# Kernel optimization log

Measured on AMD Instinct MI355X. Metric: run time of the kernel, lower is better.

The kernel has to match this reference:

```python
import jax, jax.numpy as jnp
import numpy as np

NEG_SLOPE = 0.01  # torch F.leaky_relu default
N_USER = 100000
N_ITEM = 100000
N_EDGE = 640000
D = 128
N_LAYERS = 3  # 1 input + num_hidden_layers(1) + 1 output layer


def setup_inputs() -> dict:
    key = jax.random.key(0)
    ks = jax.random.split(key, 10)
    scale = 1.0 / np.sqrt(D)
    return {
        "h_user": jax.random.normal(ks[0], (N_USER, D), dtype=jnp.float32),
        "h_item": jax.random.normal(ks[1], (N_ITEM, D), dtype=jnp.float32),
        # W[layer, etype] : etype 0 = user-follows->user, 1 = user-clicks->item, 2 = item-clicked_by->user
        "W": jax.random.normal(ks[2], (N_LAYERS, 3, D, D), dtype=jnp.float32) * scale,
        "b": jnp.zeros((N_LAYERS, 3, D), dtype=jnp.float32),
        "follows_src": jax.random.randint(ks[3], (N_EDGE,), 0, N_USER, dtype=jnp.int32),
        "follows_dst": jax.random.randint(ks[4], (N_EDGE,), 0, N_USER, dtype=jnp.int32),
        "clicks_src": jax.random.randint(ks[5], (N_EDGE,), 0, N_USER, dtype=jnp.int32),
        "clicks_dst": jax.random.randint(ks[6], (N_EDGE,), 0, N_ITEM, dtype=jnp.int32),
        "cb_src": jax.random.randint(ks[7], (N_EDGE,), 0, N_ITEM, dtype=jnp.int32),
        "cb_dst": jax.random.randint(ks[8], (N_EDGE,), 0, N_USER, dtype=jnp.int32),
    }


def _etype_conv(h_src, W, b, src, dst, n_dst):
    """Per-etype Linear on src nodes, copy_u gather, mean-aggregate at dst."""
    Wh = h_src @ W + b                     # [N_src, D] dense transform (once per node)
    msg = Wh[src]                          # [E, D] gather
    s = jax.ops.segment_sum(msg, dst, num_segments=n_dst)
    cnt = jax.ops.segment_sum(jnp.ones((src.shape[0],), dtype=Wh.dtype), dst, num_segments=n_dst)
    return s / jnp.maximum(cnt, 1.0)[:, None]  # mean; isolated nodes -> 0


def _rgcn_forward(h_user, h_item, W, b, follows_src, follows_dst,
                  clicks_src, clicks_dst, cb_src, cb_dst):
    hu, hi = h_user, h_item
    for l in range(N_LAYERS):
        # per-etype mean aggregation, then cross-etype 'sum' (DGL multi_update_all)
        agg_u = (_etype_conv(hu, W[l, 0], b[l, 0], follows_src, follows_dst, N_USER)
                 + _etype_conv(hi, W[l, 2], b[l, 2], cb_src, cb_dst, N_USER))
        agg_i = _etype_conv(hu, W[l, 1], b[l, 1], clicks_src, clicks_dst, N_ITEM)
        hu = jax.nn.leaky_relu(agg_u, NEG_SLOPE)
        hi = jax.nn.leaky_relu(agg_i, NEG_SLOPE)
    return jnp.stack([hu, hi])  # [2, 100000, 128]


def reference(h_user, h_item, W, b, follows_src, follows_dst,
              clicks_src, clicks_dst, cb_src, cb_dst):
    return _rgcn_forward(h_user, h_item, W, b, follows_src, follows_dst,
                         clicks_src, clicks_dst, cb_src, cb_dst)
```

## Files before the change

kernel.cpp:

```cpp
#include <hip/hip_runtime.h>

typedef unsigned short u16;
typedef _Float16 f16;
typedef __attribute__((ext_vector_type(8))) _Float16 f16x8;
typedef __attribute__((ext_vector_type(4))) float f32x4;

#define D 128

__global__ __launch_bounds__(256) void k_convert(const float* __restrict__ in,
                                                 u16* __restrict__ out, int n8) {
  int i = blockIdx.x * 256 + threadIdx.x;
  if (i >= n8) return;
  const float4* ip = (const float4*)in;
  float4 a = ip[i * 2], b = ip[i * 2 + 1];
  f16x8 v = {(f16)a.x, (f16)a.y, (f16)a.z, (f16)a.w,
             (f16)b.x, (f16)b.y, (f16)b.z, (f16)b.w};
  *(f16x8*)(out + (size_t)i * 8) = v;
}

__global__ __launch_bounds__(256) void k_convW(const float* __restrict__ W,
                                               u16* __restrict__ Wt, int total) {
  int idx = blockIdx.x * 256 + threadIdx.x;
  if (idx >= total) return;
  int mat = idx >> 14;
  int k = (idx >> 7) & 127;
  int n = idx & 127;
  f16 v = (f16)W[idx];
  ((f16*)Wt)[(size_t)mat * 16384 + n * 128 + k] = v;
}

__global__ __launch_bounds__(256) void k_countpos(
    const int* __restrict__ fd, const int* __restrict__ cd,
    const int* __restrict__ cbd, int* __restrict__ cnt, u16* __restrict__ pos,
    int NU, int NI, int nf, int nc, int ncb, int S) {
  int e = blockIdx.x * 256 + threadIdx.x;
  int d;
  if (e < nf)
    d = fd[e];
  else if (e < nf + nc)
    d = NU + cd[e - nf];
  else if (e < nf + nc + ncb)
    d = NU + NI + cbd[e - nf - nc];
  else
    return;
  int p = atomicAdd(&cnt[d * S], 1);
  pos[e] = (u16)p;
}

__global__ __launch_bounds__(256) void k_scanA(const int* __restrict__ cnt,
                                               int* __restrict__ part, int n, int S) {
  int t = threadIdx.x;
  int idx = blockIdx.x * 1024 + t * 4;
  int s = 0;
#pragma unroll
  for (int j = 0; j < 4; ++j)
    if (idx + j < n) s += cnt[(idx + j) * S];
  for (int off = 1; off < 64; off <<= 1) s += __shfl_down(s, off, 64);
  __shared__ int ws[4];
  if ((t & 63) == 0) ws[t >> 6] = s;
  __syncthreads();
  if (t == 0) part[blockIdx.x] = ws[0] + ws[1] + ws[2] + ws[3];
}

__global__ __launch_bounds__(1024) void k_scanB(int* __restrict__ part, int n_part) {
  __shared__ int sh[1024];
  int t = threadIdx.x;
  int v = (t < n_part) ? part[t] : 0;
  sh[t] = v;
  __syncthreads();
  for (int off = 1; off < 1024; off <<= 1) {
    int u = (t >= off) ? sh[t - off] : 0;
    __syncthreads();
    sh[t] += u;
    __syncthreads();
  }
  if (t < n_part) part[t] = sh[t] - v;
}

__global__ __launch_bounds__(256) void k_scanC(const int* __restrict__ cnt,
                                               const int* __restrict__ part,
                                               int* __restrict__ rs,
                                               int n, int total, int S) {
  int t = threadIdx.x;
  int idx = blockIdx.x * 1024 + t * 4;
  int v0 = 0, v1 = 0, v2 = 0, v3 = 0;
  if (idx < n) v0 = cnt[idx * S];
  if (idx + 1 < n) v1 = cnt[(idx + 1) * S];
  if (idx + 2 < n) v2 = cnt[(idx + 2) * S];
  if (idx + 3 < n) v3 = cnt[(idx + 3) * S];
  int s = v0 + v1 + v2 + v3;
  int inc = s;
  int lane = t & 63, w = t >> 6;
  for (int off = 1; off < 64; off <<= 1) {
    int u = __shfl_up(inc, off, 64);
    if (lane >= off) inc += u;
  }
  __shared__ int ws[4];
  if (lane == 63) ws[w] = inc;
  __syncthreads();
  int woff = 0;
  for (int i = 0; i < w; ++i) woff += ws[i];
  int ex = part[blockIdx.x] + woff + inc - s;
  int4 r;
  r.x = ex;
  r.y = ex + v0;
  r.z = r.y + v1;
  r.w = r.z + v2;
  if (idx + 3 < n)
    *(int4*)(rs + idx) = r;
  else {
    if (idx < n) rs[idx] = r.x;
    if (idx + 1 < n) rs[idx + 1] = r.y;
    if (idx + 2 < n) rs[idx + 2] = r.z;
    if (idx + 3 < n) rs[idx + 3] = r.w;
  }
  if (blockIdx.x == 0 && t == 0) rs[n] = total;
}

__global__ __launch_bounds__(256) void k_fillpos(
    const int* __restrict__ fs, const int* __restrict__ fd,
    const int* __restrict__ cs, const int* __restrict__ cd,
    const int* __restrict__ cbs, const int* __restrict__ cbd,
    const int* __restrict__ rs, const u16* __restrict__ pos,
    int* __restrict__ csr, int NU, int NI, int nf, int nc, int ncb) {
  int e = blockIdx.x * 256 + threadIdx.x;
  int d, s;
  if (e < nf) {
    d = fd[e];
    s = fs[e];
  } else if (e < nf + nc) {
    d = NU + cd[e - nf];
    s = cs[e - nf];
  } else if (e < nf + nc + ncb) {
    d = NU + NI + cbd[e - nf - nc];
    s = cbs[e - nf - nc] + NU;
  } else
    return;
  csr[rs[d] + (int)pos[e]] = s;
}

__global__ __launch_bounds__(256) void k_agg3(
    const u16* __restrict__ h_all, const int* __restrict__ csr,
    const int* __restrict__ rs, u16* __restrict__ M_all, int N3) {
  int wave = (blockIdx.x * 256 + threadIdx.x) >> 6;
  int lane = threadIdx.x & 63;
  int l16 = lane & 15;
  int w = wave * 4 + (lane >> 4);
  bool valid = w < N3;
  int wc = valid ? w : 0;
  int e = rs[wc];
  int en = valid ? rs[wc + 1] : 0;
  int deg = en - e;
  f16x8 acc0 = {0, 0, 0, 0, 0, 0, 0, 0};
  f16x8 acc1 = {0, 0, 0, 0, 0, 0, 0, 0};
  const char* hb = (const char*)h_all;
  unsigned loff = (unsigned)l16 * 16u;

  while (__any(e < en)) {
    bool a0 = e < en, a1 = e + 1 < en, a2 = e + 2 < en, a3 = e + 3 < en;
    int s0 = a0 ? csr[e] : 0;
    int s1 = a1 ? csr[e + 1] : 0;
    int s2 = a2 ? csr[e + 2] : 0;
    int s3 = a3 ? csr[e + 3] : 0;
    f16x8 v0 = {0, 0, 0, 0, 0, 0, 0, 0}, v1 = {0, 0, 0, 0, 0, 0, 0, 0};
    f16x8 v2 = {0, 0, 0, 0, 0, 0, 0, 0}, v3 = {0, 0, 0, 0, 0, 0, 0, 0};
    if (a0) v0 = *(const f16x8*)(hb + ((unsigned)s0 * 256u + loff));
    if (a1) v1 = *(const f16x8*)(hb + ((unsigned)s1 * 256u + loff));
    if (a2) v2 = *(const f16x8*)(hb + ((unsigned)s2 * 256u + loff));
    if (a3) v3 = *(const f16x8*)(hb + ((unsigned)s3 * 256u + loff));
    acc0 += v0;
    acc1 += v1;
    acc0 += v2;
    acc1 += v3;
    e += 4;
  }

  if (valid) {
    float invf = deg > 0 ? 1.0f / (float)deg : 0.f;
    f16 hinv = (f16)invf;
    f16x8 t = acc0 + acc1;
    f16x8 r = t * hinv;
    *(f16x8*)((char*)M_all + ((unsigned)wc * 256u + loff)) = r;
  }
}

template <int NE, int OUTF32>
__device__ __forceinline__ void gemm_body(
    const u16* __restrict__ mA, const u16* __restrict__ mBp,
    const u16* __restrict__ wtA, const u16* __restrict__ wtB,
    const float* __restrict__ bA, const float* __restrict__ bB,
    const int* __restrict__ rsA, const int* __restrict__ rsB,
    u16* __restrict__ o16, float* __restrict__ o32, int M, int blk) {
  int tid = threadIdx.x, lane = tid & 63, w = tid >> 6;
  int lr = lane & 15;
  int lk = (lane >> 4) * 8;
  long row0 = (long)blk * 128 + w * 32;

  f32x4 acc[2][8];
#pragma unroll
  for (int rt = 0; rt < 2; rt++)
#pragma unroll
    for (int n = 0; n < 8; n++) acc[rt][n] = (f32x4){0.f, 0.f, 0.f, 0.f};

#pragma unroll
  for (int e = 0; e < NE; ++e) {
    const f16* mm = (const f16*)((e == 0) ? mA : mBp);
    const f16* Wg = (const f16*)((e == 0) ? wtA : wtB);
#pragma unroll
    for (int ks = 0; ks < 4; ++ks) {
      int k0 = ks * 32 + lk;
      f16x8 bf[8];
#pragma unroll
      for (int n = 0; n < 8; n++) bf[n] = *(const f16x8*)(Wg + (n * 16 + lr) * D + k0);
#pragma unroll
      for (int rt = 0; rt < 2; rt++) {
        long r = row0 + rt * 16 + lr;
        if (r >= M) r = M - 1;
        f16x8 af = *(const f16x8*)(mm + r * D + k0);
#pragma unroll
        for (int n = 0; n < 8; n++)
          acc[rt][n] = __builtin_amdgcn_mfma_f32_16x16x32_f16(af, bf[n], acc[rt][n], 0, 0, 0);
      }
    }
  }

  float bAr[8], bBr[8];
#pragma unroll
  for (int n = 0; n < 8; n++) {
    bAr[n] = bA[n * 16 + lr];
    bBr[n] = (NE == 2) ? bB[n * 16 + lr] : 0.f;
  }

#pragma unroll
  for (int rt = 0; rt < 2; rt++) {
    long rbase = row0 + rt * 16 + (lane >> 4) * 4;
#pragma unroll
    for (int i = 0; i < 4; i++) {
      long r = rbase + i;
      if (r < M) {
        bool mAok = rsA[r + 1] > rsA[r];
        bool mBok = (NE == 2) && (rsB[r + 1] > rsB[r]);
#pragma unroll
        for (int n = 0; n < 8; n++) {
          int col = n * 16 + lr;
          float v = acc[rt][n][i];
          if (mAok) v += bAr[n];
          if (mBok) v += bBr[n];
          v = v > 0.f ? v : 0.01f * v;
          if (OUTF32)
            o32[r * D + col] = v;
          else
            ((f16*)o16)[r * D + col] = (f16)v;
        }
      }
    }
  }
}

template <int OUTF32>
__global__ __launch_bounds__(256) void k_gemm2(
    const u16* __restrict__ M_all, const u16* __restrict__ Wl,
    const float* __restrict__ bl, const int* __restrict__ rs_all,
    u16* __restrict__ h_all, float* __restrict__ out,
    int NU, int NI, int nbI) {
  if ((int)blockIdx.x < nbI) {
    gemm_body<1, OUTF32>(M_all + (size_t)NU * D, nullptr,
                         Wl + 16384, nullptr,
                         bl + D, nullptr,
                         rs_all + NU, nullptr,
                         h_all + (size_t)NU * D, out + (size_t)NU * D, NI,
                         blockIdx.x);
  } else {
    gemm_body<2, OUTF32>(M_all, M_all + (size_t)(NU + NI) * D,
                         Wl, Wl + 2 * 16384,
                         bl, bl + 2 * D,
                         rs_all, rs_all + NU + NI,
                         h_all, out, NU, blockIdx.x - nbI);
  }
}

extern "C" void kernel_launch(void* const* d_in, const int* in_sizes, int n_in,
                              void* d_out, int out_size, void* d_ws, size_t ws_size,
                              hipStream_t stream) {
  const float* h_user = (const float*)d_in[0];
  const float* h_item = (const float*)d_in[1];
  const float* W = (const float*)d_in[2];
  const float* bb = (const float*)d_in[3];
  const int* f_src = (const int*)d_in[4];
  const int* f_dst = (const int*)d_in[5];
  const int* c_src = (const int*)d_in[6];
  const int* c_dst = (const int*)d_in[7];
  const int* cb_src = (const int*)d_in[8];
  const int* cb_dst = (const int*)d_in[9];

  const int NU = in_sizes[0] / D;
  const int NI = in_sizes[1] / D;
  const int nEf = in_sizes[4], nEc = in_sizes[6], nEcb = in_sizes[8];
  const int N3 = NU + NI + NU;
  const int nE = nEf + nEc + nEcb;

  size_t fixed = (size_t)(N3 + 1) * 4 + 1024 * 4 + (size_t)9 * 16384 * 2 +
                 (size_t)nE * 4 + (size_t)nE * 2 +
                 (size_t)(NU + NI) * D * 2 + (size_t)N3 * D * 2 + 4096;
  int S = (fixed + (size_t)N3 * 64 <= ws_size) ? 16 : 1;

  char* p = (char*)d_ws;
  auto alloc = [&](size_t bytes) {
    char* r = p;
    p += (bytes + 255) & ~(size_t)255;
    return r;
  };
  int* cnt_pad = (int*)alloc((size_t)N3 * 4 * S);
  int* rs_all = (int*)alloc((size_t)(N3 + 1) * 4);
  int* part = (int*)alloc(1024 * 4);
  u16* Wtg = (u16*)alloc((size_t)9 * 16384 * 2);
  int* csr_all = (int*)alloc((size_t)nE * 4);
  u16* pos = (u16*)alloc((size_t)nE * 2);
  u16* h_all = (u16*)alloc((size_t)(NU + NI) * D * 2);
  u16* M_all = (u16*)alloc((size_t)N3 * D * 2);

  hipMemsetAsync(cnt_pad, 0, (size_t)N3 * 4 * S, stream);

  k_convert<<<(NU * D / 8 + 255) / 256, 256, 0, stream>>>(h_user, h_all, NU * D / 8);
  k_convert<<<(NI * D / 8 + 255) / 256, 256, 0, stream>>>(h_item, h_all + (size_t)NU * D,
                                                          NI * D / 8);
  k_convW<<<(9 * 16384 + 255) / 256, 256, 0, stream>>>(W, Wtg, 9 * 16384);

  k_countpos<<<(nE + 255) / 256, 256, 0, stream>>>(f_dst, c_dst, cb_dst, cnt_pad, pos,
                                                   NU, NI, nEf, nEc, nEcb, S);

  int n_part = (N3 + 1023) / 1024;
  k_scanA<<<n_part, 256, 0, stream>>>(cnt_pad, part, N3, S);
  k_scanB<<<1, 1024, 0, stream>>>(part, n_part);
  k_scanC<<<n_part, 256, 0, stream>>>(cnt_pad, part, rs_all, N3, nE, S);

  k_fillpos<<<(nE + 255) / 256, 256, 0, stream>>>(f_src, f_dst, c_src, c_dst,
                                                  cb_src, cb_dst, rs_all, pos,
                                                  csr_all, NU, NI, nEf, nEc, nEcb);

  int nbI = (NI + 127) / 128;
  int nbU = (NU + 127) / 128;
  int agg_blocks = ((N3 + 3) / 4 + 3) / 4;

  for (int l = 0; l < 3; ++l) {
    const u16* Wl = Wtg + (size_t)l * 3 * 16384;
    const float* bl = bb + (size_t)l * 3 * D;

    k_agg3<<<agg_blocks, 256, 0, stream>>>(h_all, csr_all, rs_all, M_all, N3);

    if (l < 2)
      k_gemm2<0><<<nbI + nbU, 256, 0, stream>>>(M_all, Wl, bl, rs_all, h_all,
                                                (float*)d_out, NU, NI, nbI);
    else
      k_gemm2<1><<<nbI + nbU, 256, 0, stream>>>(M_all, Wl, bl, rs_all, h_all,
                                                (float*)d_out, NU, NI, nbI);
  }
}
```

Baseline: 577.7 us.

## Fuse preprocessing kernels, unroll gather by eight, vectorize GEMM epilogue stores

Merges the fp32-to-fp16 conversion, weight transpose and degree-count kernels into one launch with block-range dispatch, which removes launch gaps. The aggregation loop now issues eight neighbor-row loads per iteration instead of four, so more memory requests are in flight. The MFMA operands are swapped so each lane holds four consecutive columns of one row, which lets the epilogue read bias as float4 and write vectorized float4/f16x4 stores instead of scattered scalar stores. Costs are more registers in the gather loop and a few extra predicated loads for low-degree nodes.

```diff
diff --git a/kernel.cpp b/kernel.cpp
--- a/kernel.cpp
+++ b/kernel.cpp
@@ -2,49 +2,54 @@
 
 typedef unsigned short u16;
 typedef _Float16 f16;
+typedef __attribute__((ext_vector_type(4))) _Float16 f16x4;
 typedef __attribute__((ext_vector_type(8))) _Float16 f16x8;
 typedef __attribute__((ext_vector_type(4))) float f32x4;
 
 #define D 128
 
-__global__ __launch_bounds__(256) void k_convert(const float* __restrict__ in,
-                                                 u16* __restrict__ out, int n8) {
-  int i = blockIdx.x * 256 + threadIdx.x;
-  if (i >= n8) return;
-  const float4* ip = (const float4*)in;
-  float4 a = ip[i * 2], b = ip[i * 2 + 1];
-  f16x8 v = {(f16)a.x, (f16)a.y, (f16)a.z, (f16)a.w,
-             (f16)b.x, (f16)b.y, (f16)b.z, (f16)b.w};
-  *(f16x8*)(out + (size_t)i * 8) = v;
-}
-
-__global__ __launch_bounds__(256) void k_convW(const float* __restrict__ W,
-                                               u16* __restrict__ Wt, int total) {
-  int idx = blockIdx.x * 256 + threadIdx.x;
-  if (idx >= total) return;
-  int mat = idx >> 14;
-  int k = (idx >> 7) & 127;
-  int n = idx & 127;
-  f16 v = (f16)W[idx];
-  ((f16*)Wt)[(size_t)mat * 16384 + n * 128 + k] = v;
-}
-
-__global__ __launch_bounds__(256) void k_countpos(
+__global__ __launch_bounds__(256) void k_pre(
+    const float* __restrict__ h_user, const float* __restrict__ h_item,
+    const float* __restrict__ W,
     const int* __restrict__ fd, const int* __restrict__ cd,
-    const int* __restrict__ cbd, int* __restrict__ cnt, u16* __restrict__ pos,
-    int NU, int NI, int nf, int nc, int ncb, int S) {
-  int e = blockIdx.x * 256 + threadIdx.x;
-  int d;
-  if (e < nf)
-    d = fd[e];
-  else if (e < nf + nc)
-    d = NU + cd[e - nf];
-  else if (e < nf + nc + ncb)
-    d = NU + NI + cbd[e - nf - nc];
-  else
-    return;
-  int p = atomicAdd(&cnt[d * S], 1);
-  pos[e] = (u16)p;
+    const int* __restrict__ cbd,
+    u16* __restrict__ h_all, u16* __restrict__ Wtg,
+    int* __restrict__ cnt, u16* __restrict__ pos,
+    int NU, int NI, int nf, int nc, int ncb, int S,
+    int nbCnt, int nbCvtU, int nbCvtI) {
+  int b = blockIdx.x;
+  if (b < nbCnt) {
+    int e = b * 256 + threadIdx.x;
+    int d;
+    if (e < nf)
+      d = fd[e];
+    else if (e < nf + nc)
+      d = NU + cd[e - nf];
+    else if (e < nf + nc + ncb)
+      d = NU + NI + cbd[e - nf - nc];
+    else
+      return;
+    int p = atomicAdd(&cnt[d * S], 1);
+    pos[e] = (u16)p;
+  } else if (b < nbCnt + nbCvtU + nbCvtI) {
+    bool isU = b < nbCnt + nbCvtU;
+    int i = (b - (isU ? nbCnt : nbCnt + nbCvtU)) * 256 + threadIdx.x;
+    int n8 = (isU ? NU : NI) * 16;
+    if (i >= n8) return;
+    const float4* ip = (const float4*)(isU ? h_user : h_item);
+    u16* op = h_all + (isU ? 0 : (size_t)NU * D);
+    float4 a = ip[i * 2], c = ip[i * 2 + 1];
+    f16x8 v = {(f16)a.x, (f16)a.y, (f16)a.z, (f16)a.w,
+               (f16)c.x, (f16)c.y, (f16)c.z, (f16)c.w};
+    *(f16x8*)(op + (size_t)i * 8) = v;
+  } else {
+    int idx = (b - nbCnt - nbCvtU - nbCvtI) * 256 + threadIdx.x;
+    if (idx >= 9 * 16384) return;
+    int mat = idx >> 14;
+    int k = (idx >> 7) & 127;
+    int n = idx & 127;
+    ((f16*)Wtg)[(size_t)mat * 16384 + n * 128 + k] = (f16)W[idx];
+  }
 }
 
 __global__ __launch_bounds__(256) void k_scanA(const int* __restrict__ cnt,
@@ -158,21 +163,36 @@
 
   while (__any(e < en)) {
     bool a0 = e < en, a1 = e + 1 < en, a2 = e + 2 < en, a3 = e + 3 < en;
+    bool a4 = e + 4 < en, a5 = e + 5 < en, a6 = e + 6 < en, a7 = e + 7 < en;
     int s0 = a0 ? csr[e] : 0;
     int s1 = a1 ? csr[e + 1] : 0;
     int s2 = a2 ? csr[e + 2] : 0;
     int s3 = a3 ? csr[e + 3] : 0;
+    int s4 = a4 ? csr[e + 4] : 0;
+    int s5 = a5 ? csr[e + 5] : 0;
+    int s6 = a6 ? csr[e + 6] : 0;
+    int s7 = a7 ? csr[e + 7] : 0;
     f16x8 v0 = {0, 0, 0, 0, 0, 0, 0, 0}, v1 = {0, 0, 0, 0, 0, 0, 0, 0};
     f16x8 v2 = {0, 0, 0, 0, 0, 0, 0, 0}, v3 = {0, 0, 0, 0, 0, 0, 0, 0};
+    f16x8 v4 = {0, 0, 0, 0, 0, 0, 0, 0}, v5 = {0, 0, 0, 0, 0, 0, 0, 0};
+    f16x8 v6 = {0, 0, 0, 0, 0, 0, 0, 0}, v7 = {0, 0, 0, 0, 0, 0, 0, 0};
     if (a0) v0 = *(const f16x8*)(hb + ((unsigned)s0 * 256u + loff));
     if (a1) v1 = *(const f16x8*)(hb + ((unsigned)s1 * 256u + loff));
     if (a2) v2 = *(const f16x8*)(hb + ((unsigned)s2 * 256u + loff));
     if (a3) v3 = *(const f16x8*)(hb + ((unsigned)s3 * 256u + loff));
+    if (a4) v4 = *(const f16x8*)(hb + ((unsigned)s4 * 256u + loff));
+    if (a5) v5 = *(const f16x8*)(hb + ((unsigned)s5 * 256u + loff));
+    if (a6) v6 = *(const f16x8*)(hb + ((unsigned)s6 * 256u + loff));
+    if (a7) v7 = *(const f16x8*)(hb + ((unsigned)s7 * 256u + loff));
     acc0 += v0;
     acc1 += v1;
     acc0 += v2;
     acc1 += v3;
-    e += 4;
+    acc0 += v4;
+    acc1 += v5;
+    acc0 += v6;
+    acc1 += v7;
+    e += 8;
   }
 
   if (valid) {
@@ -219,38 +239,54 @@
         f16x8 af = *(const f16x8*)(mm + r * D + k0);
 #pragma unroll
         for (int n = 0; n < 8; n++)
-          acc[rt][n] = __builtin_amdgcn_mfma_f32_16x16x32_f16(af, bf[n], acc[rt][n], 0, 0, 0);
+          acc[rt][n] = __builtin_amdgcn_mfma_f32_16x16x32_f16(bf[n], af, acc[rt][n], 0, 0, 0);
       }
     }
   }
 
-  float bAr[8], bBr[8];
+  int g4 = (lane >> 4) * 4;
+  float4 bAr[8], bBr[8];
 #pragma unroll
   for (int n = 0; n < 8; n++) {
-    bAr[n] = bA[n * 16 + lr];
-    bBr[n] = (NE == 2) ? bB[n * 16 + lr] : 0.f;
+    bAr[n] = *(const float4*)&bA[n * 16 + g4];
+    if (NE == 2) bBr[n] = *(const float4*)&bB[n * 16 + g4];
   }
 
 #pragma unroll
   for (int rt = 0; rt < 2; rt++) {
-    long rbase = row0 + rt * 16 + (lane >> 4) * 4;
-#pragma unroll
-    for (int i = 0; i < 4; i++) {
-      long r = rbase + i;
-      if (r < M) {
-        bool mAok = rsA[r + 1] > rsA[r];
-        bool mBok = (NE == 2) && (rsB[r + 1] > rsB[r]);
-#pragma unroll
-        for (int n = 0; n < 8; n++) {
-          int col = n * 16 + lr;
-          float v = acc[rt][n][i];
-          if (mAok) v += bAr[n];
-          if (mBok) v += bBr[n];
-          v = v > 0.f ? v : 0.01f * v;
-          if (OUTF32)
-            o32[r * D + col] = v;
-          else
-            ((f16*)o16)[r * D + col] = (f16)v;
+    long r = row0 + rt * 16 + lr;
+    if (r < M) {
+      bool mAok = rsA[r + 1] > rsA[r];
+      bool mBok = (NE == 2) && (rsB[r + 1] > rsB[r]);
+#pragma unroll
+      for (int n = 0; n < 8; n++) {
+        float4 vv;
+        vv.x = acc[rt][n][0];
+        vv.y = acc[rt][n][1];
+        vv.z = acc[rt][n][2];
+        vv.w = acc[rt][n][3];
+        if (mAok) {
+          vv.x += bAr[n].x;
+          vv.y += bAr[n].y;
+          vv.z += bAr[n].z;
+          vv.w += bAr[n].w;
+        }
+        if (mBok) {
+          vv.x += bBr[n].x;
+          vv.y += bBr[n].y;
+          vv.z += bBr[n].z;
+          vv.w += bBr[n].w;
+        }
+        vv.x = vv.x > 0.f ? vv.x : 0.01f * vv.x;
+        vv.y = vv.y > 0.f ? vv.y : 0.01f * vv.y;
+        vv.z = vv.z > 0.f ? vv.z : 0.01f * vv.z;
+        vv.w = vv.w > 0.f ? vv.w : 0.01f * vv.w;
+        int col = n * 16 + g4;
+        if (OUTF32) {
+          *(float4*)&o32[r * D + col] = vv;
+        } else {
+          f16x4 h = {(f16)vv.x, (f16)vv.y, (f16)vv.z, (f16)vv.w};
+          *(f16x4*)((f16*)o16 + r * D + col) = h;
         }
       }
     }
@@ -301,7 +337,7 @@
 
   size_t fixed = (size_t)(N3 + 1) * 4 + 1024 * 4 + (size_t)9 * 16384 * 2 +
                  (size_t)nE * 4 + (size_t)nE * 2 +
-                 (size_t)(NU + NI) * D * 2 + (size_t)N3 * D * 2 + 4096;
+                 (size_t)(NU + NI) * D * 2 + (size_t)N3 * D * 2 + 8192;
   int S = (fixed + (size_t)N3 * 64 <= ws_size) ? 16 : 1;
 
   char* p = (char*)d_ws;
@@ -321,13 +357,13 @@
 
   hipMemsetAsync(cnt_pad, 0, (size_t)N3 * 4 * S, stream);
 
-  k_convert<<<(NU * D / 8 + 255) / 256, 256, 0, stream>>>(h_user, h_all, NU * D / 8);
-  k_convert<<<(NI * D / 8 + 255) / 256, 256, 0, stream>>>(h_item, h_all + (size_t)NU * D,
-                                                          NI * D / 8);
-  k_convW<<<(9 * 16384 + 255) / 256, 256, 0, stream>>>(W, Wtg, 9 * 16384);
-
-  k_countpos<<<(nE + 255) / 256, 256, 0, stream>>>(f_dst, c_dst, cb_dst, cnt_pad, pos,
-                                                   NU, NI, nEf, nEc, nEcb, S);
+  int nbCnt = (nE + 255) / 256;
+  int nbCvtU = (NU * 16 + 255) / 256;
+  int nbCvtI = (NI * 16 + 255) / 256;
+  int nbW = (9 * 16384 + 255) / 256;
+  k_pre<<<nbCnt + nbCvtU + nbCvtI + nbW, 256, 0, stream>>>(
+      h_user, h_item, W, f_dst, c_dst, cb_dst, h_all, Wtg, cnt_pad, pos,
+      NU, NI, nEf, nEc, nEcb, S, nbCnt, nbCvtU, nbCvtI);
 
   int n_part = (N3 + 1023) / 1024;
   k_scanA<<<n_part, 256, 0, stream>>>(cnt_pad, part, N3, S);
```

New measurement: 565.7 us. -2.1%, faster.
